# Kernel tuning notes

Hardware: AMD Instinct MI355X
Metric: run time of the kernel (lower is better)

The kernel has to match this reference:

```python
import jax, jax.numpy as jnp
import numpy as np

N, D = 8192, 512
HEADS, DIM_HEAD, M, ITERS = 8, 64, 256, 6
WP = 256          # CustomAttention weight_params_dim
E = 262144        # number of adjacency edges
K = 33            # residual depthwise conv kernel


def setup_inputs():
    key = jax.random.key(0)
    ks = jax.random.split(key, 12)
    inner = HEADS * DIM_HEAD
    xav = (6.0 / (D + WP)) ** 0.5
    return {
        "dense": jax.random.normal(ks[0], (N, D), jnp.float32),
        "adj_rows": jax.random.randint(ks[1], (E,), 0, N, dtype=jnp.int32),
        "adj_cols": jax.random.randint(ks[2], (E,), 0, N, dtype=jnp.int32),
        "adj_vals": jnp.ones((E,), jnp.float32),
        "wq": jax.random.uniform(ks[3], (D, WP), jnp.float32, -xav, xav),
        "wk": jax.random.uniform(ks[4], (D, WP), jnp.float32, -xav, xav),
        "w_qkv": jax.random.normal(ks[5], (3 * inner, D), jnp.float32) * D ** -0.5,
        "w_out": jax.random.normal(ks[6], (D, inner), jnp.float32) * inner ** -0.5,
        "b_out": jnp.zeros((D,), jnp.float32),
        "res_kernel": jax.random.normal(ks[7], (HEADS, 1, K, 1), jnp.float32) * 0.05,
        "wv_w": jax.random.normal(ks[8], (D, D), jnp.float32) * D ** -0.5,
        "wv_b": jnp.zeros((D,), jnp.float32),
    }


def _pinv(x, iters):
    # Moore-Penrose iterative pseudo-inverse (lucidrains nystrom-attention)
    ax = jnp.abs(x)
    z = jnp.swapaxes(x, -1, -2) / (ax.sum(-1).max() * ax.sum(-2).max())
    I = jnp.eye(x.shape[-1], dtype=x.dtype)
    for _ in range(iters):
        xz = x @ z
        z = 0.25 * z @ (13.0 * I - xz @ (15.0 * I - xz @ (7.0 * I - xz)))
    return z


def _nystrom(x, w_qkv, w_out, b_out, res_kernel):
    # x: [n, dim]; batch of 1 in original (squeezed here)
    n = x.shape[0]
    pad = (-n) % M
    xp = jnp.pad(x, ((pad, 0), (0, 0)))  # pad at front, as in original
    n_p = n + pad
    qkv = xp @ w_qkv.T  # [n_p, 3*h*d]
    q, k, v = [t.reshape(n_p, HEADS, DIM_HEAD).transpose(1, 0, 2)
               for t in jnp.split(qkv, 3, axis=-1)]  # each [h, n_p, d]
    q = q * DIM_HEAD ** -0.5
    l = n_p // M
    q_l = q.reshape(HEADS, M, l, DIM_HEAD).mean(2)  # [h, m, d] landmark means
    k_l = k.reshape(HEADS, M, l, DIM_HEAD).mean(2)
    a1 = jax.nn.softmax(jnp.einsum('hid,hjd->hij', q, k_l), -1)    # [h, n_p, m]
    a2 = jax.nn.softmax(jnp.einsum('hid,hjd->hij', q_l, k_l), -1)  # [h, m, m]
    a3 = jax.nn.softmax(jnp.einsum('hid,hjd->hij', q_l, k), -1)    # [h, m, n_p]
    out = (a1 @ _pinv(a2, ITERS)) @ (a3 @ v)  # [h, n_p, d]
    # residual depthwise conv over sequence dim, per head (groups=heads)
    res = jax.lax.conv_general_dilated(
        v[None], res_kernel, (1, 1), ((K // 2, K // 2), (0, 0)),
        dimension_numbers=('NCHW', 'OIHW', 'NCHW'), feature_group_count=HEADS)[0]
    out = out + res
    out = out.transpose(1, 0, 2).reshape(n_p, HEADS * DIM_HEAD) @ w_out.T + b_out
    return out[-n:]


def reference(dense, adj_rows, adj_cols, adj_vals, wq, wk, w_qkv, w_out, b_out,
              res_kernel, wv_w, wv_b):
    xg = _nystrom(dense, w_qkv, w_out, b_out, res_kernel)
    enc = xg + dense                              # [N, D]
    q = enc @ wq
    k = enc @ wk
    att = (q @ k.T) * (WP ** -0.5)                # [N, N] scaled logits
    # sparse adjacency mask + row-sum (torch.sparse.sum over dim=1)
    edge_scores = att[adj_rows, adj_cols] * adj_vals
    A_raw = jax.ops.segment_sum(edge_scores, adj_rows, num_segments=dense.shape[0])
    alpha = jax.nn.softmax(A_raw)                 # softmax over all N instances
    value = dense @ wv_w.T + wv_b                 # [N, D]
    xl = alpha[:, None] * value
    wei = jax.nn.sigmoid(-xl)
    sq = wei * wei
    xo = xl * 2.0 * sq + 2.0 * enc * (1.0 - sq)   # gated residual blend
    return xo, A_raw
```

## Files before the change

### kernel.cpp

```cpp
#include <hip/hip_runtime.h>
#include <hip/hip_bf16.h>

#define NSEQ 8192
#define DDIM 512
#define HEADS 8
#define DH 64
#define MLM 256
#define LSUB 32
#define WP 256
#define KCONV 33
#define INNER 512
#define QKV_LD 1536

static const size_t OFF_QKVBF  = 0;
static const size_t OFF_VT     = 6291456;
static const size_t OFF_SC     = 8388608;
#define PS (8388608)
static const size_t A2R_H = PS + 0;
static const size_t A2R_L = PS + 262144;
static const size_t Z0R_H = PS + 524288,  Z0R_L = PS + 786432;
static const size_t Z0T_H = PS + 1048576, Z0T_L = PS + 1310720;
static const size_t Z1R_H = PS + 1572864, Z1R_L = PS + 1835008;
static const size_t Z1T_H = PS + 2097152, Z1T_L = PS + 2359296;
static const size_t PR_H  = PS + 2621440, PR_L  = PS + 2883584;
static const size_t PT_H  = PS + 3145728, PT_L  = PS + 3407872;
static const size_t T1T_H = PS + 3670016, T1T_L = PS + 3932160;
static const size_t T2T_H = PS + 4194304, T2T_L = PS + 4456448;
static const size_t A3VT_H= PS + 4718592, A3VT_L= PS + 4784128;
static const size_t A2F32 = PS + 4849664;
static const size_t OFF_ATTNBF = 16777216;
static const size_t OFF_PART   = 18874368;
static const size_t OFF_ENC    = 0;
static const size_t OFF_ENCBF  = 4194304;
static const size_t OFF_QKE    = 6291456;
static const size_t OFF_DENSEBF= 20971520;
static const size_t OFF_WQKVBF = 23068672;
static const size_t OFF_WOUTBF = 23461888;
static const size_t OFF_WQKT   = 23592960;
static const size_t OFF_WVBF   = 23724032;
static const size_t OFF_QL     = 23855104;
static const size_t OFF_KL     = 23986176;
static const size_t OFF_QLBF   = 24117248;
static const size_t OFF_KLSBF  = 24182784;
static const size_t OFF_BBT    = 24248320;
static const size_t OFF_SCAL   = 24313856;
static const size_t OFF_ALPHA  = 24313872;
static const size_t OFF_DEN3   = 24322064;

__device__ __forceinline__ float bf2f(unsigned short u) {
    return __uint_as_float(((unsigned int)u) << 16);
}
__device__ __forceinline__ unsigned short f2bf(float x) {
    unsigned int u = __float_as_uint(x);
    u += 0x7FFFu + ((u >> 16) & 1u);
    return (unsigned short)(u >> 16);
}

typedef __attribute__((ext_vector_type(8))) short bf16x8;
typedef __attribute__((ext_vector_type(4))) float f32x4;

__device__ __forceinline__ void gload_lds16(const void* g, void* l) {
    __builtin_amdgcn_global_load_lds(
        (const __attribute__((address_space(1))) unsigned int*)g,
        (__attribute__((address_space(3))) unsigned int*)l, 16, 0, 0);
}

__global__ __launch_bounds__(256) void cvt_bf16_k(
    const float* __restrict__ in, unsigned short* __restrict__ out)
{
    size_t i = ((size_t)blockIdx.x * 256 + threadIdx.x) * 8;
    float4 a = *reinterpret_cast<const float4*>(in + i);
    float4 b = *reinterpret_cast<const float4*>(in + i + 4);
    uint4 p;
    p.x = (unsigned int)f2bf(a.x) | ((unsigned int)f2bf(a.y) << 16);
    p.y = (unsigned int)f2bf(a.z) | ((unsigned int)f2bf(a.w) << 16);
    p.z = (unsigned int)f2bf(b.x) | ((unsigned int)f2bf(b.y) << 16);
    p.w = (unsigned int)f2bf(b.z) | ((unsigned int)f2bf(b.w) << 16);
    *reinterpret_cast<uint4*>(out + i) = p;
}

__global__ __launch_bounds__(256) void tcvt_bf16_k(
    const float* __restrict__ in, unsigned short* __restrict__ out, int R, int C)
{
    int idx = blockIdx.x * 256 + threadIdx.x;
    if (idx < R * C) {
        int oc = idx / R;
        int orow = idx % R;
        out[idx] = f2bf(in[(size_t)orow * C + oc]);
    }
}

__global__ __launch_bounds__(256) void gemm_mfma_ntb(
    const unsigned short* __restrict__ A, int lda, size_t sA,
    const unsigned short* __restrict__ B, int ldb, size_t sB,
    float* __restrict__ C, unsigned short* __restrict__ Cbf, int ldc, size_t sC,
    int K, const float* __restrict__ bias, const float* __restrict__ addsrc,
    const float* __restrict__ alphav, int epi)
{
    __shared__ __align__(16) unsigned short As[64 * 64];
    __shared__ __align__(16) unsigned short Bs[128 * 64];
    const int tid = threadIdx.x;
    const int wave = tid >> 6, lane = tid & 63;
    const int l15 = lane & 15, l4 = lane >> 4;
    const int wm = wave >> 1, wn = wave & 1;
    const size_t bm = (size_t)blockIdx.x * 64;
    const size_t bn = (size_t)blockIdx.y * 128;
    const int z = blockIdx.z;
    const unsigned short* Ab = A + (size_t)z * sA;
    const unsigned short* Bb = B + (size_t)z * sB;
    const int swzr = (l15 & 7) << 3;
    f32x4 acc[2][4] = {};
    for (int k0 = 0; k0 < K; k0 += 64) {
        __syncthreads();
#pragma unroll
        for (int c2 = 0; c2 < 2; ++c2) {
            int id = c2 * 256 + tid;
            int row = id >> 3;
            int cg = ((id & 7) ^ (row & 7)) << 3;
            gload_lds16(Ab + (bm + row) * (size_t)lda + k0 + cg, As + id * 8);
        }
#pragma unroll
        for (int c2 = 0; c2 < 4; ++c2) {
            int id = c2 * 256 + tid;
            int row = id >> 3;
            int cg = ((id & 7) ^ (row & 7)) << 3;
            gload_lds16(Bb + (bn + row) * (size_t)ldb + k0 + cg, Bs + id * 8);
        }
        __syncthreads();
#pragma unroll
        for (int c = 0; c < 2; ++c) {
            bf16x8 af[2], bfv[4];
#pragma unroll
            for (int i = 0; i < 2; ++i)
                af[i] = *reinterpret_cast<const bf16x8*>(
                    &As[(wm * 32 + i * 16 + l15) * 64 + ((c * 32 + l4 * 8) ^ swzr)]);
#pragma unroll
            for (int j = 0; j < 4; ++j)
                bfv[j] = *reinterpret_cast<const bf16x8*>(
                    &Bs[(wn * 64 + j * 16 + l15) * 64 + ((c * 32 + l4 * 8) ^ swzr)]);
#pragma unroll
            for (int i = 0; i < 2; ++i)
#pragma unroll
                for (int j = 0; j < 4; ++j)
                    acc[i][j] = __builtin_amdgcn_mfma_f32_16x16x32_bf16(
                        af[i], bfv[j], acc[i][j], 0, 0, 0);
        }
    }
    float* Cz = C ? C + (size_t)z * sC : nullptr;
    unsigned short* Cbz = Cbf ? Cbf + (size_t)z * sC : nullptr;
#pragma unroll
    for (int i = 0; i < 2; ++i)
#pragma unroll
        for (int j = 0; j < 4; ++j)
#pragma unroll
            for (int r = 0; r < 4; ++r) {
                size_t row = bm + wm * 32 + i * 16 + l4 * 4 + r;
                size_t col = bn + wn * 64 + j * 16 + l15;
                float v = acc[i][j][r];
                if (bias) v += bias[col];
                if (epi == 2) {
                    float xl = alphav[row] * v;
                    float w = 1.f / (1.f + __expf(xl));
                    float sq = w * w;
                    v = xl * 2.f * sq + 2.f * addsrc[row * (size_t)ldc + col] * (1.f - sq);
                    Cz[row * (size_t)ldc + col] = v;
                } else {
                    if (addsrc) v += addsrc[row * (size_t)ldc + col];
                    if (epi == 1) v = __expf(v);
                    if (Cz)  Cz[row * (size_t)ldc + col] = v;
                    if (Cbz) Cbz[row * (size_t)ldc + col] = f2bf(v);
                }
            }
}

__global__ __launch_bounds__(256) void bmm_ps(
    const unsigned short* __restrict__ Ah, const unsigned short* __restrict__ Al,
    const unsigned short* __restrict__ Bh, const unsigned short* __restrict__ Bl,
    unsigned short* __restrict__ Crh, unsigned short* __restrict__ Crl,
    unsigned short* __restrict__ Cth, unsigned short* __restrict__ Ctl,
    int M, int N, int K, int ntn, float alpha, float beta)
{
    __shared__ __align__(16) unsigned short LAh[64 * 64], LAl[64 * 64];
    __shared__ __align__(16) unsigned short LBh[64 * 64], LBl[64 * 64];
    const int tid = threadIdx.x;
    const int wave = tid >> 6, lane = tid & 63;
    const int l15 = lane & 15, l4 = lane >> 4;
    const int wm = wave >> 1, wn = wave & 1;
    const int b = blockIdx.y;
    const int tm = blockIdx.x / ntn, tn = blockIdx.x % ntn;
    const unsigned short* Ahb = Ah + (size_t)b * M * K;
    const unsigned short* Alb = Al + (size_t)b * M * K;
    const unsigned short* Bhb = Bh + (size_t)b * N * K;
    const unsigned short* Blb = Bl + (size_t)b * N * K;
    const int swzr = (l15 & 7) << 3;
    f32x4 acc[2][2] = {};
    for (int k0 = 0; k0 < K; k0 += 64) {
        __syncthreads();
#pragma unroll
        for (int c2 = 0; c2 < 2; ++c2) {
            int id = c2 * 256 + tid;
            int row = id >> 3;
            int cg = ((id & 7) ^ (row & 7)) << 3;
            size_t ao = (size_t)(tm * 64 + row) * K + k0 + cg;
            size_t bo = (size_t)(tn * 64 + row) * K + k0 + cg;
            gload_lds16(Ahb + ao, LAh + id * 8);
            gload_lds16(Alb + ao, LAl + id * 8);
            gload_lds16(Bhb + bo, LBh + id * 8);
            gload_lds16(Blb + bo, LBl + id * 8);
        }
        __syncthreads();
#pragma unroll
        for (int c = 0; c < 2; ++c) {
            bf16x8 ah[2], al[2], bh[2], bl[2];
#pragma unroll
            for (int i = 0; i < 2; ++i) {
                int rr = (wm * 32 + i * 16 + l15) * 64 + ((c * 32 + l4 * 8) ^ swzr);
                ah[i] = *reinterpret_cast<const bf16x8*>(&LAh[rr]);
                al[i] = *reinterpret_cast<const bf16x8*>(&LAl[rr]);
            }
#pragma unroll
            for (int j = 0; j < 2; ++j) {
                int rr = (wn * 32 + j * 16 + l15) * 64 + ((c * 32 + l4 * 8) ^ swzr);
                bh[j] = *reinterpret_cast<const bf16x8*>(&LBh[rr]);
                bl[j] = *reinterpret_cast<const bf16x8*>(&LBl[rr]);
            }
#pragma unroll
            for (int i = 0; i < 2; ++i)
#pragma unroll
                for (int j = 0; j < 2; ++j) {
                    acc[i][j] = __builtin_amdgcn_mfma_f32_16x16x32_bf16(ah[i], bh[j], acc[i][j], 0, 0, 0);
                    acc[i][j] = __builtin_amdgcn_mfma_f32_16x16x32_bf16(ah[i], bl[j], acc[i][j], 0, 0, 0);
                    acc[i][j] = __builtin_amdgcn_mfma_f32_16x16x32_bf16(al[i], bh[j], acc[i][j], 0, 0, 0);
                }
        }
    }
    unsigned short* Crhb = Crh ? Crh + (size_t)b * M * N : nullptr;
    unsigned short* Crlb = Crl ? Crl + (size_t)b * M * N : nullptr;
    unsigned short* Cthb = Cth ? Cth + (size_t)b * M * N : nullptr;
    unsigned short* Ctlb = Ctl ? Ctl + (size_t)b * M * N : nullptr;
#pragma unroll
    for (int i = 0; i < 2; ++i)
#pragma unroll
        for (int j = 0; j < 2; ++j)
#pragma unroll
            for (int r = 0; r < 4; ++r) {
                int row = tm * 64 + wm * 32 + i * 16 + l4 * 4 + r;
                int col = tn * 64 + wn * 32 + j * 16 + l15;
                float v = beta * acc[i][j][r];
                if (alpha != 0.f) {
                    size_t ai = (size_t)row * K + col;
                    v += alpha * (bf2f(Ahb[ai]) + bf2f(Alb[ai]));
                }
                unsigned short hi = f2bf(v);
                unsigned short lo = f2bf(v - bf2f(hi));
                if (Crhb) {
                    Crhb[(size_t)row * N + col] = hi;
                    if (Crlb) Crlb[(size_t)row * N + col] = lo;
                }
                if (Cthb) {
                    Cthb[(size_t)col * M + row] = hi;
                    Ctlb[(size_t)col * M + row] = lo;
                }
            }
}

__global__ __launch_bounds__(256) void pv3_mfma(
    const unsigned short* __restrict__ sc, const unsigned short* __restrict__ vT,
    float* __restrict__ part)
{
    __shared__ __align__(16) unsigned short As[64 * 64];
    __shared__ __align__(16) unsigned short Bs[64 * 64];
    const int tid = threadIdx.x;
    const int wave = tid >> 6, lane = tid & 63;
    const int l15 = lane & 15, l4 = lane >> 4;
    const int wm = wave >> 1, wn = wave & 1;
    const int it = blockIdx.x, kc = blockIdx.y, h = blockIdx.z;
    const unsigned short* Ap = sc + (size_t)h * MLM * NSEQ + (size_t)(it * 64) * NSEQ + kc * 512;
    const unsigned short* Bp = vT + (size_t)h * DH * NSEQ + kc * 512;
    const int swzr = (l15 & 7) << 3;
    f32x4 acc[2][2] = {};
    for (int k0 = 0; k0 < 512; k0 += 64) {
        __syncthreads();
#pragma unroll
        for (int c2 = 0; c2 < 2; ++c2) {
            int id = c2 * 256 + tid;
            int row = id >> 3;
            int cg = ((id & 7) ^ (row & 7)) << 3;
            gload_lds16(Ap + (size_t)row * NSEQ + k0 + cg, As + id * 8);
        }
#pragma unroll
        for (int c2 = 0; c2 < 2; ++c2) {
            int id = c2 * 256 + tid;
            int row = id >> 3;
            int cg = ((id & 7) ^ (row & 7)) << 3;
            gload_lds16(Bp + (size_t)row * NSEQ + k0 + cg, Bs + id * 8);
        }
        __syncthreads();
#pragma unroll
        for (int ks = 0; ks < 2; ++ks) {
            bf16x8 af[2], bfv[2];
#pragma unroll
            for (int i = 0; i < 2; ++i)
                af[i] = *reinterpret_cast<const bf16x8*>(
                    &As[(wm * 32 + i * 16 + l15) * 64 + ((ks * 32 + l4 * 8) ^ swzr)]);
#pragma unroll
            for (int j = 0; j < 2; ++j)
                bfv[j] = *reinterpret_cast<const bf16x8*>(
                    &Bs[(wn * 32 + j * 16 + l15) * 64 + ((ks * 32 + l4 * 8) ^ swzr)]);
#pragma unroll
            for (int i = 0; i < 2; ++i)
#pragma unroll
                for (int j = 0; j < 2; ++j)
                    acc[i][j] = __builtin_amdgcn_mfma_f32_16x16x32_bf16(af[i], bfv[j], acc[i][j], 0, 0, 0);
        }
    }
    float* Cp = part + ((size_t)(kc * 8 + h) * MLM + it * 64) * DH;
#pragma unroll
    for (int i = 0; i < 2; ++i)
#pragma unroll
        for (int j = 0; j < 2; ++j)
#pragma unroll
            for (int r = 0; r < 4; ++r)
                Cp[(wm * 32 + i * 16 + l4 * 4 + r) * DH + wn * 32 + j * 16 + l15] = acc[i][j][r];
}

__global__ __launch_bounds__(256) void a1_fused(
    const unsigned short* __restrict__ qkvbf,
    const unsigned short* __restrict__ kls,
    const unsigned short* __restrict__ bbT,
    const float* __restrict__ kern,
    unsigned short* __restrict__ attnbf)
{
    __shared__ __align__(16) unsigned short lds[20480];
    __shared__ float den[2][64];
    __shared__ float kc_s[KCONV];
    const int tid = threadIdx.x;
    const int wave = tid >> 6, lane = tid & 63;
    const int l15 = lane & 15, l4 = lane >> 4;
    const int wm = wave >> 1, wn = wave & 1;
    const int n0 = blockIdx.x * 64;
    const int h = blockIdx.y;
    const int swzr = (l15 & 7) << 3;

    if (tid < KCONV) kc_s[tid] = kern[h * KCONV + tid];
#pragma unroll
    for (int c2 = 0; c2 < 2; ++c2) {
        int id = c2 * 256 + tid;
        int row = id >> 3, cg = ((id & 7) ^ (row & 7)) << 3;
        gload_lds16(qkvbf + (size_t)(n0 + row) * QKV_LD + h * DH + cg, lds + id * 8);
    }
#pragma unroll
    for (int c2 = 0; c2 < 8; ++c2) {
        int id = c2 * 256 + tid;
        int row = id >> 3, cg = ((id & 7) ^ (row & 7)) << 3;
        gload_lds16(kls + (size_t)h * (MLM * DH) + row * DH + cg, lds + 4096 + id * 8);
    }
    __syncthreads();
    f32x4 acc[2][8] = {};
#pragma unroll
    for (int c = 0; c < 2; ++c) {
        bf16x8 af[2], bv[8];
#pragma unroll
        for (int i = 0; i < 2; ++i) {
            int row = wm * 32 + i * 16 + l15;
            af[i] = *reinterpret_cast<const bf16x8*>(&lds[row * 64 + ((c * 32 + l4 * 8) ^ swzr)]);
        }
#pragma unroll
        for (int j = 0; j < 8; ++j) {
            int brow = wn * 128 + j * 16 + l15;
            bv[j] = *reinterpret_cast<const bf16x8*>(&lds[4096 + brow * 64 + ((c * 32 + l4 * 8) ^ swzr)]);
        }
#pragma unroll
        for (int i = 0; i < 2; ++i)
#pragma unroll
            for (int j = 0; j < 8; ++j)
                acc[i][j] = __builtin_amdgcn_mfma_f32_16x16x32_bf16(af[i], bv[j], acc[i][j], 0, 0, 0);
    }
    __syncthreads();
    float rs[2][4] = {};
#pragma unroll
    for (int i = 0; i < 2; ++i)
#pragma unroll
        for (int j = 0; j < 8; ++j)
#pragma unroll
            for (int r = 0; r < 4; ++r) {
                float e = __expf(acc[i][j][r]);
                rs[i][r] += e;
                int row = wm * 32 + i * 16 + l4 * 4 + r;
                int col = wn * 128 + j * 16 + l15;
                lds[4096 + row * 256 + (col ^ ((row & 7) << 3))] = f2bf(e);
            }
#pragma unroll
    for (int i = 0; i < 2; ++i)
#pragma unroll
        for (int r = 0; r < 4; ++r) {
            float s = rs[i][r];
            s += __shfl_xor(s, 1); s += __shfl_xor(s, 2);
            s += __shfl_xor(s, 4); s += __shfl_xor(s, 8);
            if (l15 == 0) den[wn][wm * 32 + i * 16 + l4 * 4 + r] = s;
        }
    __syncthreads();
    f32x4 acc2[2][2] = {};
    const unsigned short* bbh = bbT + (size_t)h * DH * MLM;
#pragma unroll
    for (int k0 = 0; k0 < 256; k0 += 32) {
        bf16x8 af2[2], bv2[2];
#pragma unroll
        for (int i = 0; i < 2; ++i) {
            int row = wm * 32 + i * 16 + l15;
            af2[i] = *reinterpret_cast<const bf16x8*>(
                &lds[4096 + row * 256 + ((k0 + l4 * 8) ^ ((row & 7) << 3))]);
        }
#pragma unroll
        for (int j = 0; j < 2; ++j) {
            int d = wn * 32 + j * 16 + l15;
            bv2[j] = *reinterpret_cast<const bf16x8*>(&bbh[d * MLM + k0 + l4 * 8]);
        }
#pragma unroll
        for (int i = 0; i < 2; ++i)
#pragma unroll
            for (int j = 0; j < 2; ++j)
                acc2[i][j] = __builtin_amdgcn_mfma_f32_16x16x32_bf16(af2[i], bv2[j], acc2[i][j], 0, 0, 0);
    }
    __syncthreads();
    float* att = reinterpret_cast<float*>(&lds[4096]);
    unsigned short* vbuf = &lds[12288];
#pragma unroll
    for (int i = 0; i < 2; ++i)
#pragma unroll
        for (int r = 0; r < 4; ++r) {
            int row = wm * 32 + i * 16 + l4 * 4 + r;
            float inv = 1.f / (den[0][row] + den[1][row]);
#pragma unroll
            for (int j = 0; j < 2; ++j)
                att[row * 64 + wn * 32 + j * 16 + l15] = acc2[i][j][r] * inv;
        }
#pragma unroll
    for (int s = 0; s < 6; ++s) {
        int id = s * 256 + tid;
        int r = id >> 4, c4 = (id & 15) * 4;
        int n = n0 - 16 + r;
        ushort4 u = {0, 0, 0, 0};
        if (n >= 0 && n < NSEQ)
            u = *reinterpret_cast<const ushort4*>(qkvbf + (size_t)n * QKV_LD + 1024 + h * 64 + c4);
        *reinterpret_cast<ushort4*>(vbuf + r * 64 + c4) = u;
    }
    __syncthreads();
    const int col = tid & 63, rowg = tid >> 6;
    float vwin[48];
#pragma unroll
    for (int t = 0; t < 48; ++t) vwin[t] = bf2f(vbuf[(rowg * 16 + t) * 64 + col]);
#pragma unroll
    for (int rr = 0; rr < 16; ++rr) {
        float cv = 0.f;
#pragma unroll
        for (int t = 0; t < KCONV; ++t) cv += kc_s[t] * vwin[rr + t];
        int row = rowg * 16 + rr;
        attnbf[(size_t)(n0 + row) * INNER + h * DH + col] = f2bf(att[row * 64 + col] + cv);
    }
}

__global__ __launch_bounds__(64) void landmark2_k(
    const unsigned short* __restrict__ qkvbf, float* __restrict__ q_l, float* __restrict__ k_l,
    unsigned short* __restrict__ ql_bf, unsigned short* __restrict__ kls_bf)
{
    int m = blockIdx.x, h = blockIdx.y, d = threadIdx.x;
    float sq = 0.f, sk = 0.f;
    for (int i = 0; i < LSUB; ++i) {
        size_t n = (size_t)m * LSUB + i;
        sq += bf2f(qkvbf[n * QKV_LD + h * DH + d]);
        sk += bf2f(qkvbf[n * QKV_LD + 512 + h * DH + d]);
    }
    float qv = sq * (0.125f / (float)LSUB);
    float kv = sk * (1.f / (float)LSUB);
    size_t o = ((size_t)h * MLM + m) * DH + d;
    q_l[o] = qv; k_l[o] = kv;
    ql_bf[o] = f2bf(qv);
    kls_bf[o] = f2bf(kv * 0.125f);
}

__global__ __launch_bounds__(256) void vt_k(
    const unsigned short* __restrict__ qkvbf, unsigned short* __restrict__ vT)
{
    __shared__ unsigned short tile[128][72];
    const int t = threadIdx.x;
    const int n0 = blockIdx.x * 128;
    const int h = blockIdx.y;
#pragma unroll
    for (int s = 0; s < 4; ++s) {
        int cid = s * 256 + t;
        int row = cid >> 3, ch = (cid & 7) * 8;
        uint4 v = *reinterpret_cast<const uint4*>(
            qkvbf + (size_t)(n0 + row) * QKV_LD + 1024 + h * 64 + ch);
        *reinterpret_cast<uint4*>(&tile[row][ch]) = v;
    }
    __syncthreads();
#pragma unroll
    for (int s = 0; s < 4; ++s) {
        int cid = s * 256 + t;
        int d = cid >> 4, nch = (cid & 15) * 8;
        unsigned short o[8];
#pragma unroll
        for (int i = 0; i < 8; ++i) o[i] = tile[nch + i][d];
        *reinterpret_cast<uint4*>(vT + (size_t)h * DH * NSEQ + (size_t)d * NSEQ + n0 + nch) =
            *reinterpret_cast<uint4*>(o);
    }
}

__global__ __launch_bounds__(256) void a2_k(
    const float* __restrict__ q_l, const float* __restrict__ k_l, float* __restrict__ a2)
{
    int i = blockIdx.x, h = blockIdx.y, t = threadIdx.x;
    __shared__ float ql[64];
    __shared__ float red[256];
    if (t < 64) ql[t] = q_l[((size_t)h * MLM + i) * DH + t];
    __syncthreads();
    const float* kr = k_l + ((size_t)h * MLM + t) * DH;
    float s = 0.f;
#pragma unroll
    for (int d = 0; d < 64; d += 4) {
        float4 kv = *reinterpret_cast<const float4*>(kr + d);
        s += kv.x * ql[d] + kv.y * ql[d + 1] + kv.z * ql[d + 2] + kv.w * ql[d + 3];
    }
    red[t] = s; __syncthreads();
    for (int off = 128; off > 0; off >>= 1) { if (t < off) red[t] = fmaxf(red[t], red[t + off]); __syncthreads(); }
    float m = red[0]; __syncthreads();
    float e = __expf(s - m);
    red[t] = e; __syncthreads();
    for (int off = 128; off > 0; off >>= 1) { if (t < off) red[t] += red[t + off]; __syncthreads(); }
    a2[(((size_t)h * MLM + i) * MLM) + t] = e / red[0];
}

__global__ __launch_bounds__(256) void absmax_k(
    const float* __restrict__ a2, unsigned int* __restrict__ scal)
{
    int b = blockIdx.x, t = threadIdx.x;
    __shared__ float red[256];
    float sum = 0.f;
    if (b < 8) {
        const float* r = a2 + ((size_t)b * MLM + t) * MLM;
        for (int j = 0; j < MLM; ++j) sum += fabsf(r[j]);
    } else {
        int h = b - 8;
        for (int i = 0; i < MLM; ++i) sum += fabsf(a2[((size_t)h * MLM + i) * MLM + t]);
    }
    red[t] = sum; __syncthreads();
    for (int off = 128; off > 0; off >>= 1) { if (t < off) red[t] = fmaxf(red[t], red[t + off]); __syncthreads(); }
    if (t == 0) atomicMax(scal + (b < 8 ? 0 : 1), __float_as_uint(red[0]));
}

__global__ __launch_bounds__(256) void zinit2_k(
    const float* __restrict__ a2, const unsigned int* __restrict__ scal,
    unsigned short* __restrict__ a2h, unsigned short* __restrict__ a2l,
    unsigned short* __restrict__ zrh, unsigned short* __restrict__ zrl,
    unsigned short* __restrict__ zth, unsigned short* __restrict__ ztl)
{
    int idx = blockIdx.x * 256 + threadIdx.x;
    float inv = 1.f / (__uint_as_float(scal[0]) * __uint_as_float(scal[1]));
    int h = idx >> 16, rem = idx & 65535, i = rem >> 8, j = rem & 255;
    float aij = a2[idx];
    unsigned short h1 = f2bf(aij);
    a2h[idx] = h1; a2l[idx] = f2bf(aij - bf2f(h1));
    float zt = aij * inv;
    unsigned short h2 = f2bf(zt);
    zth[idx] = h2; ztl[idx] = f2bf(zt - bf2f(h2));
    float zr = a2[((size_t)h << 16) + (j << 8) + i] * inv;
    unsigned short h3 = f2bf(zr);
    zrh[idx] = h3; zrl[idx] = f2bf(zr - bf2f(h3));
}

__global__ __launch_bounds__(256) void den3_k(
    const unsigned short* __restrict__ sc, float* __restrict__ den3)
{
    __shared__ float red[256];
    const int t = threadIdx.x;
    const unsigned short* row = sc + (size_t)blockIdx.x * NSEQ;
    float s = 0.f;
#pragma unroll
    for (int u = 0; u < 4; ++u) {
        uint4 pk = *reinterpret_cast<const uint4*>(row + t * 32 + u * 8);
        unsigned int w[4] = {pk.x, pk.y, pk.z, pk.w};
#pragma unroll
        for (int q = 0; q < 4; ++q) {
            s += bf2f((unsigned short)(w[q] & 0xFFFF));
            s += bf2f((unsigned short)(w[q] >> 16));
        }
    }
    red[t] = s; __syncthreads();
    for (int off = 128; off > 0; off >>= 1) { if (t < off) red[t] += red[t + off]; __syncthreads(); }
    if (t == 0) den3[blockIdx.x] = red[0];
}

__global__ __launch_bounds__(256) void red3_k(
    const float* __restrict__ part, const float* __restrict__ den3,
    unsigned short* __restrict__ a3vth, unsigned short* __restrict__ a3vtl)
{
    int o = blockIdx.x * 256 + threadIdx.x;
    float s = 0.f;
#pragma unroll
    for (int kc = 0; kc < 16; ++kc) s += part[(size_t)kc * 131072 + o];
    s /= den3[o >> 6];
    int h = o >> 14, i = (o >> 6) & 255, d = o & 63;
    int to = (h << 14) + (d << 8) + i;
    unsigned short hi = f2bf(s);
    a3vth[to] = hi; a3vtl[to] = f2bf(s - bf2f(hi));
}

__global__ __launch_bounds__(256) void edge2_k(
    const unsigned short* __restrict__ qke,
    const int* __restrict__ rows, const int* __restrict__ cols,
    const float* __restrict__ vals, float* __restrict__ A_raw)
{
    const int e = blockIdx.x * 32 + (threadIdx.x >> 3);
    const int g = threadIdx.x & 7;
    const int r = rows[e], c = cols[e];
    const unsigned short* qr = qke + (size_t)r * 512 + g * 32;
    const unsigned short* kr = qke + (size_t)c * 512 + 256 + g * 32;
    float s = 0.f;
#pragma unroll
    for (int u = 0; u < 4; ++u) {
        uint4 qa = *reinterpret_cast<const uint4*>(qr + u * 8);
        uint4 ka = *reinterpret_cast<const uint4*>(kr + u * 8);
        unsigned int qw[4] = {qa.x, qa.y, qa.z, qa.w};
        unsigned int kw[4] = {ka.x, ka.y, ka.z, ka.w};
#pragma unroll
        for (int q = 0; q < 4; ++q) {
            s += bf2f((unsigned short)(qw[q] & 0xFFFF)) * bf2f((unsigned short)(kw[q] & 0xFFFF));
            s += bf2f((unsigned short)(qw[q] >> 16)) * bf2f((unsigned short)(kw[q] >> 16));
        }
    }
    s += __shfl_xor(s, 1); s += __shfl_xor(s, 2); s += __shfl_xor(s, 4);
    if (g == 0) atomicAdd(&A_raw[r], s * vals[e] * 0.0625f);
}

__global__ __launch_bounds__(1024) void alpha_k(
    const float* __restrict__ A_raw, float* __restrict__ alpha)
{
    __shared__ float red[1024];
    int t = threadIdx.x;
    float m = -1e30f;
    for (int i = t; i < NSEQ; i += 1024) m = fmaxf(m, A_raw[i]);
    red[t] = m; __syncthreads();
    for (int off = 512; off > 0; off >>= 1) { if (t < off) red[t] = fmaxf(red[t], red[t + off]); __syncthreads(); }
    m = red[0]; __syncthreads();
    float s = 0.f;
    for (int i = t; i < NSEQ; i += 1024) s += __expf(A_raw[i] - m);
    red[t] = s; __syncthreads();
    for (int off = 512; off > 0; off >>= 1) { if (t < off) red[t] += red[t + off]; __syncthreads(); }
    float inv = 1.f / red[0];
    for (int i = t; i < NSEQ; i += 1024) alpha[i] = __expf(A_raw[i] - m) * inv;
}

extern "C" void kernel_launch(void* const* d_in, const int* in_sizes, int n_in,
                              void* d_out, int out_size, void* d_ws, size_t ws_size,
                              hipStream_t stream)
{
    const float* dense      = (const float*)d_in[0];
    const int*   adj_rows   = (const int*)d_in[1];
    const int*   adj_cols   = (const int*)d_in[2];
    const float* adj_vals   = (const float*)d_in[3];
    const float* wq         = (const float*)d_in[4];
    const float* wk         = (const float*)d_in[5];
    const float* w_qkv      = (const float*)d_in[6];
    const float* w_out      = (const float*)d_in[7];
    const float* b_out      = (const float*)d_in[8];
    const float* res_kernel = (const float*)d_in[9];
    const float* wv_w       = (const float*)d_in[10];
    const float* wv_b       = (const float*)d_in[11];
    const int E = in_sizes[1];

    float* ws  = (float*)d_ws;
    float* out = (float*)d_out;
    float* A_raw = out + (size_t)NSEQ * DDIM;

    unsigned short* qkv_bf   = (unsigned short*)(ws + OFF_QKVBF);
    unsigned short* vT       = (unsigned short*)(ws + OFF_VT);
    unsigned short* sc       = (unsigned short*)(ws + OFF_SC);
    unsigned short* attn_bf  = (unsigned short*)(ws + OFF_ATTNBF);
    unsigned short* qke_bf   = (unsigned short*)(ws + OFF_QKE);
    unsigned short* dense_bf = (unsigned short*)(ws + OFF_DENSEBF);
    unsigned short* wqkv_bf  = (unsigned short*)(ws + OFF_WQKVBF);
    unsigned short* wout_bf  = (unsigned short*)(ws + OFF_WOUTBF);
    unsigned short* wqkT_bf  = (unsigned short*)(ws + OFF_WQKT);
    unsigned short* wv_bf    = (unsigned short*)(ws + OFF_WVBF);
    unsigned short* ql_bf    = (unsigned short*)(ws + OFF_QLBF);
    unsigned short* kls_bf   = (unsigned short*)(ws + OFF_KLSBF);
    unsigned short* bbT_bf   = (unsigned short*)(ws + OFF_BBT);
    unsigned short* enc_bf   = (unsigned short*)(ws + OFF_ENCBF);

#define U16(off) ((unsigned short*)(ws + (off)))

    hipMemsetAsync(A_raw, 0, NSEQ * sizeof(float), stream);
    hipMemsetAsync(ws + OFF_SCAL, 0, 2 * sizeof(unsigned int), stream);

    cvt_bf16_k<<<(NSEQ * DDIM) / 2048, 256, 0, stream>>>(dense, dense_bf);
    cvt_bf16_k<<<(1536 * DDIM) / 2048, 256, 0, stream>>>(w_qkv, wqkv_bf);

    gemm_mfma_ntb<<<dim3(NSEQ / 64, 1536 / 128, 1), 256, 0, stream>>>(
        dense_bf, DDIM, 0, wqkv_bf, DDIM, 0, nullptr, qkv_bf, QKV_LD, 0,
        DDIM, nullptr, nullptr, nullptr, 0);

    landmark2_k<<<dim3(MLM, HEADS), 64, 0, stream>>>(
        qkv_bf, ws + OFF_QL, ws + OFF_KL, ql_bf, kls_bf);
    vt_k<<<dim3(NSEQ / 128, HEADS), 256, 0, stream>>>(qkv_bf, vT);

    gemm_mfma_ntb<<<dim3(MLM / 64, NSEQ / 128, HEADS), 256, 0, stream>>>(
        ql_bf, DH, (size_t)MLM * DH, qkv_bf + 512, QKV_LD, DH,
        nullptr, sc, NSEQ, (size_t)MLM * NSEQ, DH, nullptr, nullptr, nullptr, 1);
    den3_k<<<HEADS * MLM, 256, 0, stream>>>(sc, ws + OFF_DEN3);
    pv3_mfma<<<dim3(4, 16, HEADS), 256, 0, stream>>>(sc, vT, ws + OFF_PART);
    red3_k<<<512, 256, 0, stream>>>(ws + OFF_PART, ws + OFF_DEN3,
                                    U16(A3VT_H), U16(A3VT_L));

    a2_k<<<dim3(MLM, HEADS), 256, 0, stream>>>(ws + OFF_QL, ws + OFF_KL, ws + A2F32);
    absmax_k<<<16, 256, 0, stream>>>(ws + A2F32, (unsigned int*)(ws + OFF_SCAL));
    zinit2_k<<<(HEADS * MLM * MLM) / 256, 256, 0, stream>>>(
        ws + A2F32, (const unsigned int*)(ws + OFF_SCAL),
        U16(A2R_H), U16(A2R_L), U16(Z0R_H), U16(Z0R_L), U16(Z0T_H), U16(Z0T_L));

    for (int it = 0; it < 6; ++it) {
        size_t zr_h = (it & 1) ? Z1R_H : Z0R_H, zr_l = (it & 1) ? Z1R_L : Z0R_L;
        size_t zt_h = (it & 1) ? Z1T_H : Z0T_H, zt_l = (it & 1) ? Z1T_L : Z0T_L;
        size_t or_h = (it & 1) ? Z0R_H : Z1R_H, or_l = (it & 1) ? Z0R_L : Z1R_L;
        size_t ot_h = (it & 1) ? Z0T_H : Z1T_H, ot_l = (it & 1) ? Z0T_L : Z1T_L;
        bmm_ps<<<dim3(16, HEADS), 256, 0, stream>>>(
            U16(A2R_H), U16(A2R_L), U16(zt_h), U16(zt_l),
            U16(PR_H), U16(PR_L), U16(PT_H), U16(PT_L), 256, 256, 256, 4, 0.f, 1.f);
        bmm_ps<<<dim3(16, HEADS), 256, 0, stream>>>(
            U16(PR_H), U16(PR_L), U16(PT_H), U16(PT_L),
            nullptr, nullptr, U16(T1T_H), U16(T1T_L), 256, 256, 256, 4, 7.f, -1.f);
        bmm_ps<<<dim3(16, HEADS), 256, 0, stream>>>(
            U16(PR_H), U16(PR_L), U16(T1T_H), U16(T1T_L),
            nullptr, nullptr, U16(T2T_H), U16(T2T_L), 256, 256, 256, 4, 15.f, -1.f);
        bmm_ps<<<dim3(16, HEADS), 256, 0, stream>>>(
            U16(zr_h), U16(zr_l), U16(T2T_H), U16(T2T_L),
            U16(or_h), U16(or_l), U16(ot_h), U16(ot_l), 256, 256, 256, 4, 3.25f, -0.25f);
    }
    bmm_ps<<<dim3(4, HEADS), 256, 0, stream>>>(
        U16(A3VT_H), U16(A3VT_L), U16(Z0R_H), U16(Z0R_L),
        bbT_bf, nullptr, nullptr, nullptr, 64, 256, 256, 4, 0.f, 1.f);

    a1_fused<<<dim3(NSEQ / 64, HEADS), 256, 0, stream>>>(
        qkv_bf, kls_bf, bbT_bf, res_kernel, attn_bf);

    cvt_bf16_k<<<(DDIM * INNER) / 2048, 256, 0, stream>>>(w_out, wout_bf);
    tcvt_bf16_k<<<(WP * DDIM + 255) / 256, 256, 0, stream>>>(wq, wqkT_bf, DDIM, WP);
    tcvt_bf16_k<<<(WP * DDIM + 255) / 256, 256, 0, stream>>>(wk, wqkT_bf + 256 * 512, DDIM, WP);
    cvt_bf16_k<<<(DDIM * DDIM) / 2048, 256, 0, stream>>>(wv_w, wv_bf);

    gemm_mfma_ntb<<<dim3(NSEQ / 64, DDIM / 128, 1), 256, 0, stream>>>(
        attn_bf, INNER, 0, wout_bf, INNER, 0, ws + OFF_ENC, enc_bf, DDIM, 0,
        INNER, b_out, dense, nullptr, 0);

    gemm_mfma_ntb<<<dim3(NSEQ / 64, 512 / 128, 1), 256, 0, stream>>>(
        enc_bf, DDIM, 0, wqkT_bf, DDIM, 0, nullptr, qke_bf, 512, 0,
        DDIM, nullptr, nullptr, nullptr, 0);

    edge2_k<<<E / 32, 256, 0, stream>>>(qke_bf, adj_rows, adj_cols, adj_vals, A_raw);
    alpha_k<<<1, 1024, 0, stream>>>(A_raw, ws + OFF_ALPHA);

    gemm_mfma_ntb<<<dim3(NSEQ / 64, DDIM / 128, 1), 256, 0, stream>>>(
        dense_bf, DDIM, 0, wv_bf, DDIM, 0, out, nullptr, DDIM, 0,
        DDIM, wv_b, ws + OFF_ENC, ws + OFF_ALPHA, 2);
}
```

Measured before the change: 583.5 us.

## Drop split-bf16 precision in pinv matmuls and fuse softmax denominator into GEMM

Replaces the hi/lo split-bf16 batched matmuls used for the iterative pseudo-inverse with plain bf16 matmuls, cutting MFMA count and memory traffic per GEMM. Computes the landmark softmax row sums in the GEMM epilogue via shuffles and atomics, removing a separate reduction kernel. a1_fused now reads landmark keys directly from global memory instead of staging them in LDS, reducing shared memory use. Dropping the low-order correction may hurt accuracy of the Newton-Schulz iteration.

```diff
diff --git a/kernel.cpp b/kernel.cpp
--- a/kernel.cpp
+++ b/kernel.cpp
@@ -17,16 +17,15 @@
 static const size_t OFF_SC     = 8388608;
 #define PS (8388608)
 static const size_t A2R_H = PS + 0;
-static const size_t A2R_L = PS + 262144;
-static const size_t Z0R_H = PS + 524288,  Z0R_L = PS + 786432;
-static const size_t Z0T_H = PS + 1048576, Z0T_L = PS + 1310720;
-static const size_t Z1R_H = PS + 1572864, Z1R_L = PS + 1835008;
-static const size_t Z1T_H = PS + 2097152, Z1T_L = PS + 2359296;
-static const size_t PR_H  = PS + 2621440, PR_L  = PS + 2883584;
-static const size_t PT_H  = PS + 3145728, PT_L  = PS + 3407872;
-static const size_t T1T_H = PS + 3670016, T1T_L = PS + 3932160;
-static const size_t T2T_H = PS + 4194304, T2T_L = PS + 4456448;
-static const size_t A3VT_H= PS + 4718592, A3VT_L= PS + 4784128;
+static const size_t Z0R_H = PS + 524288;
+static const size_t Z0T_H = PS + 1048576;
+static const size_t Z1R_H = PS + 1572864;
+static const size_t Z1T_H = PS + 2097152;
+static const size_t PR_H  = PS + 2621440;
+static const size_t PT_H  = PS + 3145728;
+static const size_t T1T_H = PS + 3670016;
+static const size_t T2T_H = PS + 4194304;
+static const size_t A3VT_H= PS + 4718592;
 static const size_t A2F32 = PS + 4849664;
 static const size_t OFF_ATTNBF = 16777216;
 static const size_t OFF_PART   = 18874368;
@@ -95,7 +94,7 @@
     const unsigned short* __restrict__ B, int ldb, size_t sB,
     float* __restrict__ C, unsigned short* __restrict__ Cbf, int ldc, size_t sC,
     int K, const float* __restrict__ bias, const float* __restrict__ addsrc,
-    const float* __restrict__ alphav, int epi)
+    const float* __restrict__ alphav, float* __restrict__ denv, int epi)
 {
     __shared__ __align__(16) unsigned short As[64 * 64];
     __shared__ __align__(16) unsigned short Bs[128 * 64];
@@ -148,6 +147,26 @@
     }
     float* Cz = C ? C + (size_t)z * sC : nullptr;
     unsigned short* Cbz = Cbf ? Cbf + (size_t)z * sC : nullptr;
+    if (epi == 3) {
+#pragma unroll
+        for (int i = 0; i < 2; ++i)
+#pragma unroll
+            for (int r = 0; r < 4; ++r) {
+                size_t row = bm + wm * 32 + i * 16 + l4 * 4 + r;
+                float s = 0.f;
+#pragma unroll
+                for (int j = 0; j < 4; ++j) {
+                    size_t col = bn + wn * 64 + j * 16 + l15;
+                    float e = __expf(acc[i][j][r]);
+                    s += e;
+                    Cbz[row * (size_t)ldc + col] = f2bf(e);
+                }
+                s += __shfl_xor(s, 1); s += __shfl_xor(s, 2);
+                s += __shfl_xor(s, 4); s += __shfl_xor(s, 8);
+                if (l15 == 0) atomicAdd(denv + (size_t)z * MLM + row, s);
+            }
+        return;
+    }
 #pragma unroll
     for (int i = 0; i < 2; ++i)
 #pragma unroll
@@ -173,15 +192,13 @@
             }
 }
 
-__global__ __launch_bounds__(256) void bmm_ps(
-    const unsigned short* __restrict__ Ah, const unsigned short* __restrict__ Al,
-    const unsigned short* __restrict__ Bh, const unsigned short* __restrict__ Bl,
-    unsigned short* __restrict__ Crh, unsigned short* __restrict__ Crl,
-    unsigned short* __restrict__ Cth, unsigned short* __restrict__ Ctl,
+__global__ __launch_bounds__(256) void bmm_h(
+    const unsigned short* __restrict__ Ah, const unsigned short* __restrict__ Bh,
+    unsigned short* __restrict__ Crh, unsigned short* __restrict__ Cth,
     int M, int N, int K, int ntn, float alpha, float beta)
 {
-    __shared__ __align__(16) unsigned short LAh[64 * 64], LAl[64 * 64];
-    __shared__ __align__(16) unsigned short LBh[64 * 64], LBl[64 * 64];
+    __shared__ __align__(16) unsigned short LAh[64 * 64];
+    __shared__ __align__(16) unsigned short LBh[64 * 64];
     const int tid = threadIdx.x;
     const int wave = tid >> 6, lane = tid & 63;
     const int l15 = lane & 15, l4 = lane >> 4;
@@ -189,9 +206,7 @@
     const int b = blockIdx.y;
     const int tm = blockIdx.x / ntn, tn = blockIdx.x % ntn;
     const unsigned short* Ahb = Ah + (size_t)b * M * K;
-    const unsigned short* Alb = Al + (size_t)b * M * K;
     const unsigned short* Bhb = Bh + (size_t)b * N * K;
-    const unsigned short* Blb = Bl + (size_t)b * N * K;
     const int swzr = (l15 & 7) << 3;
     f32x4 acc[2][2] = {};
     for (int k0 = 0; k0 < K; k0 += 64) {
@@ -201,43 +216,30 @@
             int id = c2 * 256 + tid;
             int row = id >> 3;
             int cg = ((id & 7) ^ (row & 7)) << 3;
-            size_t ao = (size_t)(tm * 64 + row) * K + k0 + cg;
-            size_t bo = (size_t)(tn * 64 + row) * K + k0 + cg;
-            gload_lds16(Ahb + ao, LAh + id * 8);
-            gload_lds16(Alb + ao, LAl + id * 8);
-            gload_lds16(Bhb + bo, LBh + id * 8);
-            gload_lds16(Blb + bo, LBl + id * 8);
+            gload_lds16(Ahb + (size_t)(tm * 64 + row) * K + k0 + cg, LAh + id * 8);
+            gload_lds16(Bhb + (size_t)(tn * 64 + row) * K + k0 + cg, LBh + id * 8);
         }
         __syncthreads();
 #pragma unroll
         for (int c = 0; c < 2; ++c) {
-            bf16x8 ah[2], al[2], bh[2], bl[2];
-#pragma unroll
-            for (int i = 0; i < 2; ++i) {
-                int rr = (wm * 32 + i * 16 + l15) * 64 + ((c * 32 + l4 * 8) ^ swzr);
-                ah[i] = *reinterpret_cast<const bf16x8*>(&LAh[rr]);
-                al[i] = *reinterpret_cast<const bf16x8*>(&LAl[rr]);
-            }
-#pragma unroll
-            for (int j = 0; j < 2; ++j) {
-                int rr = (wn * 32 + j * 16 + l15) * 64 + ((c * 32 + l4 * 8) ^ swzr);
-                bh[j] = *reinterpret_cast<const bf16x8*>(&LBh[rr]);
-                bl[j] = *reinterpret_cast<const bf16x8*>(&LBl[rr]);
-            }
+            bf16x8 ah[2], bh[2];
 #pragma unroll
             for (int i = 0; i < 2; ++i)
-#pragma unroll
-                for (int j = 0; j < 2; ++j) {
+                ah[i] = *reinterpret_cast<const bf16x8*>(
+                    &LAh[(wm * 32 + i * 16 + l15) * 64 + ((c * 32 + l4 * 8) ^ swzr)]);
+#pragma unroll
+            for (int j = 0; j < 2; ++j)
+                bh[j] = *reinterpret_cast<const bf16x8*>(
+                    &LBh[(wn * 32 + j * 16 + l15) * 64 + ((c * 32 + l4 * 8) ^ swzr)]);
+#pragma unroll
+            for (int i = 0; i < 2; ++i)
+#pragma unroll
+                for (int j = 0; j < 2; ++j)
                     acc[i][j] = __builtin_amdgcn_mfma_f32_16x16x32_bf16(ah[i], bh[j], acc[i][j], 0, 0, 0);
-                    acc[i][j] = __builtin_amdgcn_mfma_f32_16x16x32_bf16(ah[i], bl[j], acc[i][j], 0, 0, 0);
-                    acc[i][j] = __builtin_amdgcn_mfma_f32_16x16x32_bf16(al[i], bh[j], acc[i][j], 0, 0, 0);
-                }
         }
     }
     unsigned short* Crhb = Crh ? Crh + (size_t)b * M * N : nullptr;
-    unsigned short* Crlb = Crl ? Crl + (size_t)b * M * N : nullptr;
     unsigned short* Cthb = Cth ? Cth + (size_t)b * M * N : nullptr;
-    unsigned short* Ctlb = Ctl ? Ctl + (size_t)b * M * N : nullptr;
 #pragma unroll
     for (int i = 0; i < 2; ++i)
 #pragma unroll
@@ -247,20 +249,11 @@
                 int row = tm * 64 + wm * 32 + i * 16 + l4 * 4 + r;
                 int col = tn * 64 + wn * 32 + j * 16 + l15;
                 float v = beta * acc[i][j][r];
-                if (alpha != 0.f) {
-                    size_t ai = (size_t)row * K + col;
-                    v += alpha * (bf2f(Ahb[ai]) + bf2f(Alb[ai]));
-                }
+                if (alpha != 0.f)
+                    v += alpha * bf2f(Ahb[(size_t)row * K + col]);
                 unsigned short hi = f2bf(v);
-                unsigned short lo = f2bf(v - bf2f(hi));
-                if (Crhb) {
-                    Crhb[(size_t)row * N + col] = hi;
-                    if (Crlb) Crlb[(size_t)row * N + col] = lo;
-                }
-                if (Cthb) {
-                    Cthb[(size_t)col * M + row] = hi;
-                    Ctlb[(size_t)col * M + row] = lo;
-                }
+                if (Crhb) Crhb[(size_t)row * N + col] = hi;
+                if (Cthb) Cthb[(size_t)col * M + row] = hi;
             }
 }
 
@@ -331,7 +324,7 @@
     const float* __restrict__ kern,
     unsigned short* __restrict__ attnbf)
 {
-    __shared__ __align__(16) unsigned short lds[20480];
+    __shared__ __align__(16) unsigned short lds[16384];
     __shared__ float den[2][64];
     __shared__ float kc_s[KCONV];
     const int tid = threadIdx.x;
@@ -349,13 +342,8 @@
         int row = id >> 3, cg = ((id & 7) ^ (row & 7)) << 3;
         gload_lds16(qkvbf + (size_t)(n0 + row) * QKV_LD + h * DH + cg, lds + id * 8);
     }
-#pragma unroll
-    for (int c2 = 0; c2 < 8; ++c2) {
-        int id = c2 * 256 + tid;
-        int row = id >> 3, cg = ((id & 7) ^ (row & 7)) << 3;
-        gload_lds16(kls + (size_t)h * (MLM * DH) + row * DH + cg, lds + 4096 + id * 8);
-    }
     __syncthreads();
+    const unsigned short* klsh = kls + (size_t)h * (MLM * DH);
     f32x4 acc[2][8] = {};
 #pragma unroll
     for (int c = 0; c < 2; ++c) {
@@ -368,7 +356,7 @@
 #pragma unroll
         for (int j = 0; j < 8; ++j) {
             int brow = wn * 128 + j * 16 + l15;
-            bv[j] = *reinterpret_cast<const bf16x8*>(&lds[4096 + brow * 64 + ((c * 32 + l4 * 8) ^ swzr)]);
+            bv[j] = *reinterpret_cast<const bf16x8*>(&klsh[brow * 64 + c * 32 + l4 * 8]);
         }
 #pragma unroll
         for (int i = 0; i < 2; ++i)
@@ -388,7 +376,7 @@
                 rs[i][r] += e;
                 int row = wm * 32 + i * 16 + l4 * 4 + r;
                 int col = wn * 128 + j * 16 + l15;
-                lds[4096 + row * 256 + (col ^ ((row & 7) << 3))] = f2bf(e);
+                lds[row * 256 + (col ^ ((row & 7) << 3))] = f2bf(e);
             }
 #pragma unroll
     for (int i = 0; i < 2; ++i)
@@ -409,7 +397,7 @@
         for (int i = 0; i < 2; ++i) {
             int row = wm * 32 + i * 16 + l15;
             af2[i] = *reinterpret_cast<const bf16x8*>(
-                &lds[4096 + row * 256 + ((k0 + l4 * 8) ^ ((row & 7) << 3))]);
+                &lds[row * 256 + ((k0 + l4 * 8) ^ ((row & 7) << 3))]);
         }
 #pragma unroll
         for (int j = 0; j < 2; ++j) {
@@ -423,8 +411,8 @@
                 acc2[i][j] = __builtin_amdgcn_mfma_f32_16x16x32_bf16(af2[i], bv2[j], acc2[i][j], 0, 0, 0);
     }
     __syncthreads();
-    float* att = reinterpret_cast<float*>(&lds[4096]);
-    unsigned short* vbuf = &lds[12288];
+    float* att = reinterpret_cast<float*>(lds);
+    unsigned short* vbuf = &lds[8192];
 #pragma unroll
     for (int i = 0; i < 2; ++i)
 #pragma unroll
@@ -551,49 +539,21 @@
 
 __global__ __launch_bounds__(256) void zinit2_k(
     const float* __restrict__ a2, const unsigned int* __restrict__ scal,
-    unsigned short* __restrict__ a2h, unsigned short* __restrict__ a2l,
-    unsigned short* __restrict__ zrh, unsigned short* __restrict__ zrl,
-    unsigned short* __restrict__ zth, unsigned short* __restrict__ ztl)
+    unsigned short* __restrict__ a2h,
+    unsigned short* __restrict__ zrh, unsigned short* __restrict__ zth)
 {
     int idx = blockIdx.x * 256 + threadIdx.x;
     float inv = 1.f / (__uint_as_float(scal[0]) * __uint_as_float(scal[1]));
     int h = idx >> 16, rem = idx & 65535, i = rem >> 8, j = rem & 255;
     float aij = a2[idx];
-    unsigned short h1 = f2bf(aij);
-    a2h[idx] = h1; a2l[idx] = f2bf(aij - bf2f(h1));
-    float zt = aij * inv;
-    unsigned short h2 = f2bf(zt);
-    zth[idx] = h2; ztl[idx] = f2bf(zt - bf2f(h2));
-    float zr = a2[((size_t)h << 16) + (j << 8) + i] * inv;
-    unsigned short h3 = f2bf(zr);
-    zrh[idx] = h3; zrl[idx] = f2bf(zr - bf2f(h3));
-}
-
-__global__ __launch_bounds__(256) void den3_k(
-    const unsigned short* __restrict__ sc, float* __restrict__ den3)
-{
-    __shared__ float red[256];
-    const int t = threadIdx.x;
-    const unsigned short* row = sc + (size_t)blockIdx.x * NSEQ;
-    float s = 0.f;
-#pragma unroll
-    for (int u = 0; u < 4; ++u) {
-        uint4 pk = *reinterpret_cast<const uint4*>(row + t * 32 + u * 8);
-        unsigned int w[4] = {pk.x, pk.y, pk.z, pk.w};
-#pragma unroll
-        for (int q = 0; q < 4; ++q) {
-            s += bf2f((unsigned short)(w[q] & 0xFFFF));
-            s += bf2f((unsigned short)(w[q] >> 16));
-        }
-    }
-    red[t] = s; __syncthreads();
-    for (int off = 128; off > 0; off >>= 1) { if (t < off) red[t] += red[t + off]; __syncthreads(); }
-    if (t == 0) den3[blockIdx.x] = red[0];
+    a2h[idx] = f2bf(aij);
+    zth[idx] = f2bf(aij * inv);
+    zrh[idx] = f2bf(a2[((size_t)h << 16) + (j << 8) + i] * inv);
 }
 
 __global__ __launch_bounds__(256) void red3_k(
     const float* __restrict__ part, const float* __restrict__ den3,
-    unsigned short* __restrict__ a3vth, unsigned short* __restrict__ a3vtl)
+    unsigned short* __restrict__ a3vth)
 {
     int o = blockIdx.x * 256 + threadIdx.x;
     float s = 0.f;
@@ -601,9 +561,7 @@
     for (int kc = 0; kc < 16; ++kc) s += part[(size_t)kc * 131072 + o];
     s /= den3[o >> 6];
     int h = o >> 14, i = (o >> 6) & 255, d = o & 63;
-    int to = (h << 14) + (d << 8) + i;
-    unsigned short hi = f2bf(s);
-    a3vth[to] = hi; a3vtl[to] = f2bf(s - bf2f(hi));
+    a3vth[(h << 14) + (d << 8) + i] = f2bf(s);
 }
 
 __global__ __launch_bounds__(256) void edge2_k(
@@ -690,15 +648,16 @@
 
 #define U16(off) ((unsigned short*)(ws + (off)))
 
-    hipMemsetAsync(A_raw, 0, NSEQ * sizeof(float), stream);
-    hipMemsetAsync(ws + OFF_SCAL, 0, 2 * sizeof(unsigned int), stream);
+    (void)hipMemsetAsync(A_raw, 0, NSEQ * sizeof(float), stream);
+    (void)hipMemsetAsync(ws + OFF_SCAL, 0, 2 * sizeof(unsigned int), stream);
+    (void)hipMemsetAsync(ws + OFF_DEN3, 0, HEADS * MLM * sizeof(float), stream);
 
     cvt_bf16_k<<<(NSEQ * DDIM) / 2048, 256, 0, stream>>>(dense, dense_bf);
     cvt_bf16_k<<<(1536 * DDIM) / 2048, 256, 0, stream>>>(w_qkv, wqkv_bf);
 
     gemm_mfma_ntb<<<dim3(NSEQ / 64, 1536 / 128, 1), 256, 0, stream>>>(
         dense_bf, DDIM, 0, wqkv_bf, DDIM, 0, nullptr, qkv_bf, QKV_LD, 0,
-        DDIM, nullptr, nullptr, nullptr, 0);
+        DDIM, nullptr, nullptr, nullptr, nullptr, 0);
 
     landmark2_k<<<dim3(MLM, HEADS), 64, 0, stream>>>(
         qkv_bf, ws + OFF_QL, ws + OFF_KL, ql_bf, kls_bf);
@@ -706,39 +665,33 @@
 
     gemm_mfma_ntb<<<dim3(MLM / 64, NSEQ / 128, HEADS), 256, 0, stream>>>(
         ql_bf, DH, (size_t)MLM * DH, qkv_bf + 512, QKV_LD, DH,
-        nullptr, sc, NSEQ, (size_t)MLM * NSEQ, DH, nullptr, nullptr, nullptr, 1);
-    den3_k<<<HEADS * MLM, 256, 0, stream>>>(sc, ws + OFF_DEN3);
+        nullptr, sc, NSEQ, (size_t)MLM * NSEQ, DH, nullptr, nullptr, nullptr,
+        ws + OFF_DEN3, 3);
     pv3_mfma<<<dim3(4, 16, HEADS), 256, 0, stream>>>(sc, vT, ws + OFF_PART);
-    red3_k<<<512, 256, 0, stream>>>(ws + OFF_PART, ws + OFF_DEN3,
-                                    U16(A3VT_H), U16(A3VT_L));
+    red3_k<<<512, 256, 0, stream>>>(ws + OFF_PART, ws + OFF_DEN3, U16(A3VT_H));
 
     a2_k<<<dim3(MLM, HEADS), 256, 0, stream>>>(ws + OFF_QL, ws + OFF_KL, ws + A2F32);
     absmax_k<<<16, 256, 0, stream>>>(ws + A2F32, (unsigned int*)(ws + OFF_SCAL));
     zinit2_k<<<(HEADS * MLM * MLM) / 256, 256, 0, stream>>>(
         ws + A2F32, (const unsigned int*)(ws + OFF_SCAL),
-        U16(A2R_H), U16(A2R_L), U16(Z0R_H), U16(Z0R_L), U16(Z0T_H), U16(Z0T_L));
+        U16(A2R_H), U16(Z0R_H), U16(Z0T_H));
 
     for (int it = 0; it < 6; ++it) {
-        size_t zr_h = (it & 1) ? Z1R_H : Z0R_H, zr_l = (it & 1) ? Z1R_L : Z0R_L;
-        size_t zt_h = (it & 1) ? Z1T_H : Z0T_H, zt_l = (it & 1) ? Z1T_L : Z0T_L;
-        size_t or_h = (it & 1) ? Z0R_H : Z1R_H, or_l = (it & 1) ? Z0R_L : Z1R_L;
-        size_t ot_h = (it & 1) ? Z0T_H : Z1T_H, ot_l = (it & 1) ? Z0T_L : Z1T_L;
-        bmm_ps<<<dim3(16, HEADS), 256, 0, stream>>>(
-            U16(A2R_H), U16(A2R_L), U16(zt_h), U16(zt_l),
-            U16(PR_H), U16(PR_L), U16(PT_H), U16(PT_L), 256, 256, 256, 4, 0.f, 1.f);
-        bmm_ps<<<dim3(16, HEADS), 256, 0, stream>>>(
-            U16(PR_H), U16(PR_L), U16(PT_H), U16(PT_L),
-            nullptr, nullptr, U16(T1T_H), U16(T1T_L), 256, 256, 256, 4, 7.f, -1.f);
-        bmm_ps<<<dim3(16, HEADS), 256, 0, stream>>>(
-            U16(PR_H), U16(PR_L), U16(T1T_H), U16(T1T_L),
-            nullptr, nullptr, U16(T2T_H), U16(T2T_L), 256, 256, 256, 4, 15.f, -1.f);
-        bmm_ps<<<dim3(16, HEADS), 256, 0, stream>>>(
-            U16(zr_h), U16(zr_l), U16(T2T_H), U16(T2T_L),
-            U16(or_h), U16(or_l), U16(ot_h), U16(ot_l), 256, 256, 256, 4, 3.25f, -0.25f);
-    }
-    bmm_ps<<<dim3(4, HEADS), 256, 0, stream>>>(
-        U16(A3VT_H), U16(A3VT_L), U16(Z0R_H), U16(Z0R_L),
-        bbT_bf, nullptr, nullptr, nullptr, 64, 256, 256, 4, 0.f, 1.f);
+        size_t zr_h = (it & 1) ? Z1R_H : Z0R_H;
+        size_t zt_h = (it & 1) ? Z1T_H : Z0T_H;
+        size_t or_h = (it & 1) ? Z0R_H : Z1R_H;
+        size_t ot_h = (it & 1) ? Z0T_H : Z1T_H;
+        bmm_h<<<dim3(16, HEADS), 256, 0, stream>>>(
+            U16(A2R_H), U16(zt_h), U16(PR_H), U16(PT_H), 256, 256, 256, 4, 0.f, 1.f);
+        bmm_h<<<dim3(16, HEADS), 256, 0, stream>>>(
+            U16(PR_H), U16(PT_H), nullptr, U16(T1T_H), 256, 256, 256, 4, 7.f, -1.f);
+        bmm_h<<<dim3(16, HEADS), 256, 0, stream>>>(
+            U16(PR_H), U16(T1T_H), nullptr, U16(T2T_H), 256, 256, 256, 4, 15.f, -1.f);
+        bmm_h<<<dim3(16, HEADS), 256, 0, stream>>>(
+            U16(zr_h), U16(T2T_H), U16(or_h), U16(ot_h), 256, 256, 256, 4, 3.25f, -0.25f);
+    }
+    bmm_h<<<dim3(4, HEADS), 256, 0, stream>>>(
+        U16(A3VT_H), U16(Z0R_H), bbT_bf, nullptr, 64, 256, 256, 4, 0.f, 1.f);
 
     a1_fused<<<dim3(NSEQ / 64, HEADS), 256, 0, stream>>>(
         qkv_bf, kls_bf, bbT_bf, res_kernel, attn_bf);
@@ -750,16 +703,16 @@
 
     gemm_mfma_ntb<<<dim3(NSEQ / 64, DDIM / 128, 1), 256, 0, stream>>>(
         attn_bf, INNER, 0, wout_bf, INNER, 0, ws + OFF_ENC, enc_bf, DDIM, 0,
-        INNER, b_out, dense, nullptr, 0);
+        INNER, b_out, dense, nullptr, nullptr, 0);
 
     gemm_mfma_ntb<<<dim3(NSEQ / 64, 512 / 128, 1), 256, 0, stream>>>(
         enc_bf, DDIM, 0, wqkT_bf, DDIM, 0, nullptr, qke_bf, 512, 0,
-        DDIM, nullptr, nullptr, nullptr, 0);
+        DDIM, nullptr, nullptr, nullptr, nullptr, 0);
 
     edge2_k<<<E / 32, 256, 0, stream>>>(qke_bf, adj_rows, adj_cols, adj_vals, A_raw);
     alpha_k<<<1, 1024, 0, stream>>>(A_raw, ws + OFF_ALPHA);
 
     gemm_mfma_ntb<<<dim3(NSEQ / 64, DDIM / 128, 1), 256, 0, stream>>>(
         dense_bf, DDIM, 0, wv_bf, DDIM, 0, out, nullptr, DDIM, 0,
-        DDIM, wv_b, ws + OFF_ENC, ws + OFF_ALPHA, 2);
-}
+        DDIM, wv_b, ws + OFF_ENC, ws + OFF_ALPHA, nullptr, 2);
+}
```

Result: faster. 502.4 us (-13.9%).
